# Kernel tuning notes

Measured on AMD Instinct MI355X. Metric: run time of the kernel, lower is better.

Reference implementation:

```python
import jax, jax.numpy as jnp
import numpy as np

N = 50000      # nodes
E = 800000     # edges (avg degree 16)
IN, HID, OUT = 256, 128, 64


def _glorot(key, shape):
    fan_in, fan_out = shape[0], shape[1]
    limit = np.sqrt(6.0 / (fan_in + fan_out))
    return jax.random.uniform(key, shape, jnp.float32, -limit, limit)


def setup_inputs() -> dict:
    key = jax.random.key(0)
    ks = jax.random.split(key, 8)
    x = jax.random.normal(ks[0], (N, IN), jnp.float32)
    edge_index = jax.random.randint(ks[1], (2, E), 0, N, dtype=jnp.int64)
    W1 = _glorot(ks[2], (IN, HID))
    b1 = jnp.zeros((HID,), jnp.float32)
    W2 = _glorot(ks[3], (HID, OUT))
    b2 = jnp.zeros((OUT,), jnp.float32)
    aw1 = _glorot(ks[4], (HID, 1))
    ab1 = jnp.zeros((1,), jnp.float32)
    aw2 = _glorot(ks[5], (OUT, 1))
    ab2 = jnp.zeros((1,), jnp.float32)
    return {"x": x, "edge_index": edge_index, "W1": W1, "b1": b1,
            "W2": W2, "b2": b2, "aw1": aw1, "ab1": ab1, "aw2": aw2, "ab2": ab2}


def gcn_conv(x, W, b, src, dst, n):
    # PyG GCNConv: add self-loops, symmetric degree normalization, then aggregate.
    h = x @ W                                   # [n, out]
    loops = jnp.arange(n, dtype=src.dtype)
    s = jnp.concatenate([src, loops])           # [E+n]
    d = jnp.concatenate([dst, loops])
    deg = jax.ops.segment_sum(jnp.ones(s.shape[0], h.dtype), d, num_segments=n)
    dinv = jnp.where(deg > 0, jax.lax.rsqrt(deg), 0.0)
    norm = dinv[s] * dinv[d]                    # [E+n]
    out = jax.ops.segment_sum(h[s] * norm[:, None], d, num_segments=n)
    return out + b


def reference(x, edge_index, W1, b1, W2, b2, aw1, ab1, aw2, ab2):
    # eval mode: dropout is identity
    src, dst = edge_index[0], edge_index[1]
    h = gcn_conv(x, W1, b1, src, dst, N)
    h = jax.nn.relu(h)
    h = h * jax.nn.sigmoid(h @ aw1 + ab1)       # sigmoid attention gate 1
    h = gcn_conv(h, W2, b2, src, dst, N)
    return h * jax.nn.sigmoid(h @ aw2 + ab2)    # sigmoid attention gate 2
```

## Files before the change

### kernel.cpp

```cpp
#include <hip/hip_runtime.h>
#include <math.h>

#define N_NODES 50000
#define N_EDGES 800000
#define D_IN    256
#define D_HID   128
#define D_OUT   64

#define NB 196
#define CH 2048
#define SLAB 4608

typedef unsigned int u32;
typedef unsigned short u16;
typedef __attribute__((ext_vector_type(8))) short bf16x8;
typedef __attribute__((ext_vector_type(4))) float f32x4;

__device__ __forceinline__ float bflo(u32 u) {
    union { u32 i; float f; } c; c.i = u << 16; return c.f;
}
__device__ __forceinline__ float bfhi(u32 u) {
    union { u32 i; float f; } c; c.i = u & 0xffff0000u; return c.f;
}
__device__ __forceinline__ u32 pack_bf2(float a, float b) {
    union { float f; u32 i; } ca, cb; ca.f = a; cb.f = b;
    u32 ra = (ca.i + 0x7fffu + ((ca.i >> 16) & 1u)) >> 16;
    u32 rb = (cb.i + 0x7fffu + ((cb.i >> 16) & 1u)) & 0xffff0000u;
    return ra | rb;
}

__device__ __forceinline__ int edge_at(const void* ei, int is64, int which, int i) {
    if (is64) return (int)((const long long*)ei)[(size_t)which * N_EDGES + i];
    return ((const int*)ei)[which * N_EDGES + i];
}

__device__ __forceinline__ int detect_is64(const void* ei, int t, int* s_is32) {
    if (t == 0) *s_is32 = 0;
    __syncthreads();
    if (t < 256) {
        int vv = ((const int*)ei)[2 * t + 1];
        if (vv != 0) atomicOr(s_is32, 1);
    }
    __syncthreads();
    return (*s_is32 == 0);
}


__global__ __launch_bounds__(256) void k_scatter1(const void* __restrict__ ei,
                                                  int* __restrict__ bcur,
                                                  u32* __restrict__ ebuf) {
    __shared__ int h[NB], gbase[NB], lc[NB];
    __shared__ int s_is32;
    int t = threadIdx.x;
    int is64 = detect_is64(ei, t, &s_is32);
    for (int i = t; i < NB; i += 256) { h[i] = 0; lc[i] = 0; }
    __syncthreads();
    int base = blockIdx.x * CH;

    u32 p[CH / 256];
    #pragma unroll
    for (int j = 0; j < CH / 256; ++j) {
        int i = base + j * 256 + t;
        if (i < N_EDGES) {
            int s = edge_at(ei, is64, 0, i);
            int d = edge_at(ei, is64, 1, i);
            p[j] = (u32)s | ((u32)d << 16);
            atomicAdd(&h[d >> 8], 1);
        }
    }
    __syncthreads();
    for (int i = t; i < NB; i += 256) if (h[i]) gbase[i] = atomicAdd(&bcur[i], h[i]);
    __syncthreads();
    #pragma unroll
    for (int j = 0; j < CH / 256; ++j) {
        int i = base + j * 256 + t;
        if (i < N_EDGES) {
            int b = (int)(p[j] >> 24);
            int lp = atomicAdd(&lc[b], 1);
            ebuf[gbase[b] + lp] = p[j];
        }
    }
}

__global__ __launch_bounds__(256) void k_scatter2(const u32* __restrict__ ebuf,
                                                  const int* __restrict__ bcur,
                                                  int* __restrict__ rowstart,
                                                  int* __restrict__ cnt,
                                                  float* __restrict__ dinv,
                                                  int* __restrict__ colidx) {
    __shared__ int h2[256], lofs[256], cur[256], sm[256];
    int b = blockIdx.x, t = threadIdx.x;
    int e0 = b * SLAB, ne = bcur[b] - e0;
    h2[t] = 0; cur[t] = 0;
    __syncthreads();
    for (int i = t; i < ne; i += 256) {
        u32 p = ebuf[e0 + i];
        atomicAdd(&h2[(p >> 16) & 255], 1);
    }
    __syncthreads();
    int v = h2[t]; sm[t] = v; __syncthreads();
    for (int off = 1; off < 256; off <<= 1) {
        int a = (t >= off) ? sm[t - off] : 0;
        __syncthreads();
        sm[t] += a;
        __syncthreads();
    }
    lofs[t] = sm[t] - v;
    __syncthreads();
    int node = (b << 8) + t;
    if (node < N_NODES) {
        rowstart[node] = e0 + lofs[t];
        cnt[node] = v;
        dinv[node] = rsqrtf(1.0f + (float)v);
    }
    for (int i = t; i < ne; i += 256) {
        u32 p = ebuf[e0 + i];
        int dl = (p >> 16) & 255;
        int lp = atomicAdd(&cur[dl], 1);
        colidx[e0 + lofs[dl] + lp] = (int)(p & 0xffffu);
    }
}

__global__ void k_wsplit(const float* __restrict__ W1, u16* __restrict__ t1h,
                         u16* __restrict__ t1l, const float* __restrict__ W2,
                         u16* __restrict__ t2h, u16* __restrict__ t2l,
                         int* __restrict__ bcur) {
    int i = blockIdx.x * 256 + threadIdx.x;
    if (i < NB) bcur[i] = i * SLAB;
    if (i < D_IN * D_HID) {
        int k = i / D_HID, c = i - k * D_HID;
        u32 bits = __float_as_uint(W1[i]);
        u32 hb = bits & 0xffff0000u;
        float lo = __uint_as_float(bits) - __uint_as_float(hb);
        t1h[(size_t)c * D_IN + k] = (u16)(hb >> 16);
        t1l[(size_t)c * D_IN + k] = (u16)(__float_as_uint(lo) >> 16);
    }
    int j = i - D_IN * D_HID;
    if (j >= 0 && j < D_HID * D_OUT) {
        int k = j / D_OUT, c = j - k * D_OUT;
        u32 bits = __float_as_uint(W2[j]);
        u32 hb = bits & 0xffff0000u;
        float lo = __uint_as_float(bits) - __uint_as_float(hb);
        t2h[(size_t)c * D_HID + k] = (u16)(hb >> 16);
        t2l[(size_t)c * D_HID + k] = (u16)(__float_as_uint(lo) >> 16);
    }
}

template <int K, int NF>
__global__ __launch_bounds__(256) void k_gemm_mfma(
    const float* __restrict__ A, const u16* __restrict__ tHi,
    const u16* __restrict__ tLo, const float* __restrict__ dinv,
    u32* __restrict__ Cp, int M) {
    constexpr int NT = NF / 16;
    constexpr int LDK = 40;
    __shared__ u16 aH[128][LDK], aL[128][LDK];
    __shared__ u16 wH[NF][LDK], wL[NF][LDK];

    const int t = threadIdx.x;
    const int lane = t & 63, wv = t >> 6;
    const int m0 = blockIdx.x * 128;
    const int lr = lane & 15, lk = (lane >> 4) * 8;

    f32x4 acc[2][NT] = {};

    const int arow = t >> 1;
    const int akq = (t & 1) * 16;
    const bool aok = (m0 + arow) < M;
    const float* asrc = A + (size_t)(m0 + arow) * K + akq;

    for (int ks = 0; ks < K; ks += 32) {
        {
            float f[16];
            #pragma unroll
            for (int j = 0; j < 16; ++j) f[j] = 0.0f;
            if (aok) {
                const float4* p = (const float4*)(asrc + ks);
                float4 v0 = p[0], v1 = p[1], v2 = p[2], v3 = p[3];
                f[0] = v0.x; f[1] = v0.y; f[2]  = v0.z; f[3]  = v0.w;
                f[4] = v1.x; f[5] = v1.y; f[6]  = v1.z; f[7]  = v1.w;
                f[8] = v2.x; f[9] = v2.y; f[10] = v2.z; f[11] = v2.w;
                f[12] = v3.x; f[13] = v3.y; f[14] = v3.z; f[15] = v3.w;
            }
            u32 hp[8], lp[8];
            #pragma unroll
            for (int q = 0; q < 8; ++q) {
                u32 b0 = __float_as_uint(f[2 * q]);
                u32 b1 = __float_as_uint(f[2 * q + 1]);
                u32 h0 = b0 & 0xffff0000u, h1 = b1 & 0xffff0000u;
                float l0 = f[2 * q] - __uint_as_float(h0);
                float l1 = f[2 * q + 1] - __uint_as_float(h1);
                hp[q] = (h0 >> 16) | h1;
                lp[q] = (__float_as_uint(l0) >> 16) | (__float_as_uint(l1) & 0xffff0000u);
            }
            *(uint4*)&aH[arow][akq + 0] = make_uint4(hp[0], hp[1], hp[2], hp[3]);
            *(uint4*)&aH[arow][akq + 8] = make_uint4(hp[4], hp[5], hp[6], hp[7]);
            *(uint4*)&aL[arow][akq + 0] = make_uint4(lp[0], lp[1], lp[2], lp[3]);
            *(uint4*)&aL[arow][akq + 8] = make_uint4(lp[4], lp[5], lp[6], lp[7]);
        }
        #pragma unroll
        for (int idx = t; idx < NF * 4; idx += 256) {
            int col = idx >> 2;
            int k8 = (idx & 3) * 8;
            *(uint4*)&wH[col][k8] = *(const uint4*)&tHi[(size_t)col * K + ks + k8];
            *(uint4*)&wL[col][k8] = *(const uint4*)&tLo[(size_t)col * K + ks + k8];
        }
        __syncthreads();

        bf16x8 afH[2], afL[2];
        #pragma unroll
        for (int mt = 0; mt < 2; ++mt) {
            int r = wv * 32 + mt * 16 + lr;
            afH[mt] = *(const bf16x8*)&aH[r][lk];
            afL[mt] = *(const bf16x8*)&aL[r][lk];
        }
        #pragma unroll
        for (int nt = 0; nt < NT; ++nt) {
            bf16x8 bh = *(const bf16x8*)&wH[nt * 16 + lr][lk];
            bf16x8 bl = *(const bf16x8*)&wL[nt * 16 + lr][lk];
            #pragma unroll
            for (int mt = 0; mt < 2; ++mt) {
                acc[mt][nt] = __builtin_amdgcn_mfma_f32_16x16x32_bf16(afH[mt], bh, acc[mt][nt], 0, 0, 0);
                acc[mt][nt] = __builtin_amdgcn_mfma_f32_16x16x32_bf16(afL[mt], bh, acc[mt][nt], 0, 0, 0);
                acc[mt][nt] = __builtin_amdgcn_mfma_f32_16x16x32_bf16(afH[mt], bl, acc[mt][nt], 0, 0, 0);
            }
        }
        __syncthreads();
    }

    #pragma unroll
    for (int mt = 0; mt < 2; ++mt) {
        #pragma unroll
        for (int r = 0; r < 4; ++r) {
            int row = m0 + wv * 32 + mt * 16 + (lane >> 4) * 4 + r;
            float dv = (row < M) ? dinv[row] : 0.0f;
            #pragma unroll
            for (int nt = 0; nt < NT; ++nt) {
                float v = acc[mt][nt][r] * dv;
                float vn = __shfl_xor(v, 1);
                if (!(lane & 1) && row < M) {
                    Cp[(size_t)row * (NF / 2) + nt * 8 + (lr >> 1)] = pack_bf2(v, vn);
                }
            }
        }
    }
}


__global__ __launch_bounds__(256) void k_agg1(
        const u32* __restrict__ hs, const int* __restrict__ rowstart,
        const int* __restrict__ cnt, const int* __restrict__ colidx,
        const float* __restrict__ dinv,
        const float* __restrict__ b, const float* __restrict__ aw,
        const float* __restrict__ ab, float* __restrict__ out) {
    int v = blockIdx.x * 4 + (threadIdx.x >> 6);
    int l = threadIdx.x & 63;
    if (v >= N_NODES) return;
    float dv = dinv[v];
    u32 su = hs[(size_t)v * 64 + l];
    float ax = bflo(su), ay = bfhi(su);
    int start = rowstart[v], len = cnt[v];
    const int* cx = colidx + start;
    int j = 0;
    for (; j + 8 <= len; j += 8) {
        int s0 = cx[j], s1 = cx[j + 1], s2 = cx[j + 2], s3 = cx[j + 3];
        int s4 = cx[j + 4], s5 = cx[j + 5], s6 = cx[j + 6], s7 = cx[j + 7];
        u32 u0 = hs[(size_t)s0 * 64 + l];
        u32 u1 = hs[(size_t)s1 * 64 + l];
        u32 u2 = hs[(size_t)s2 * 64 + l];
        u32 u3 = hs[(size_t)s3 * 64 + l];
        u32 u4 = hs[(size_t)s4 * 64 + l];
        u32 u5 = hs[(size_t)s5 * 64 + l];
        u32 u6 = hs[(size_t)s6 * 64 + l];
        u32 u7 = hs[(size_t)s7 * 64 + l];
        ax += bflo(u0) + bflo(u1) + bflo(u2) + bflo(u3)
            + bflo(u4) + bflo(u5) + bflo(u6) + bflo(u7);
        ay += bfhi(u0) + bfhi(u1) + bfhi(u2) + bfhi(u3)
            + bfhi(u4) + bfhi(u5) + bfhi(u6) + bfhi(u7);
    }
    for (; j + 4 <= len; j += 4) {
        int s0 = cx[j], s1 = cx[j + 1], s2 = cx[j + 2], s3 = cx[j + 3];
        u32 u0 = hs[(size_t)s0 * 64 + l];
        u32 u1 = hs[(size_t)s1 * 64 + l];
        u32 u2 = hs[(size_t)s2 * 64 + l];
        u32 u3 = hs[(size_t)s3 * 64 + l];
        ax += bflo(u0) + bflo(u1) + bflo(u2) + bflo(u3);
        ay += bfhi(u0) + bfhi(u1) + bfhi(u2) + bfhi(u3);
    }
    for (; j < len; ++j) {
        u32 u = hs[(size_t)cx[j] * 64 + l];
        ax += bflo(u); ay += bfhi(u);
    }
    float2 bp = ((const float2*)b)[l];
    ax = fmaxf(ax * dv + bp.x, 0.0f);
    ay = fmaxf(ay * dv + bp.y, 0.0f);
    float2 ap = ((const float2*)aw)[l];
    float p = ax * ap.x + ay * ap.y;
    for (int off = 32; off; off >>= 1) p += __shfl_xor(p, off);
    float g = 1.0f / (1.0f + expf(-(p + ab[0])));
    ((float2*)out)[(size_t)v * 64 + l] = make_float2(ax * g, ay * g);
}

__global__ __launch_bounds__(256) void k_agg2(
        const u32* __restrict__ hs, const int* __restrict__ rowstart,
        const int* __restrict__ cnt, const int* __restrict__ colidx,
        const float* __restrict__ dinv,
        const float* __restrict__ b, const float* __restrict__ aw,
        const float* __restrict__ ab, float* __restrict__ out) {
    int v = blockIdx.x * 4 + (threadIdx.x >> 6);
    int l = threadIdx.x & 63;
    if (v >= N_NODES) return;
    int c = l & 31, half = l >> 5;
    float dv = dinv[v];
    float ax = 0.0f, ay = 0.0f;
    if (half == 0) {
        u32 su = hs[(size_t)v * 32 + c];
        ax = bflo(su); ay = bfhi(su);
    }
    int start = rowstart[v], len = cnt[v];
    const int* cx = colidx + start;
    int j = half;
    for (; j + 6 < len; j += 8) {
        int s0 = cx[j], s1 = cx[j + 2], s2 = cx[j + 4], s3 = cx[j + 6];
        u32 u0 = hs[(size_t)s0 * 32 + c];
        u32 u1 = hs[(size_t)s1 * 32 + c];
        u32 u2 = hs[(size_t)s2 * 32 + c];
        u32 u3 = hs[(size_t)s3 * 32 + c];
        ax += bflo(u0) + bflo(u1) + bflo(u2) + bflo(u3);
        ay += bfhi(u0) + bfhi(u1) + bfhi(u2) + bfhi(u3);
    }
    for (; j + 2 < len; j += 4) {
        int s0 = cx[j], s1 = cx[j + 2];
        u32 u0 = hs[(size_t)s0 * 32 + c];
        u32 u1 = hs[(size_t)s1 * 32 + c];
        ax += bflo(u0) + bflo(u1);
        ay += bfhi(u0) + bfhi(u1);
    }
    if (j < len) {
        u32 u = hs[(size_t)cx[j] * 32 + c];
        ax += bflo(u); ay += bfhi(u);
    }
    ax += __shfl_xor(ax, 32);
    ay += __shfl_xor(ay, 32);
    float2 bp = ((const float2*)b)[c];
    ax = ax * dv + bp.x;
    ay = ay * dv + bp.y;
    float2 ap = ((const float2*)aw)[c];
    float p = ax * ap.x + ay * ap.y;
    for (int off = 16; off; off >>= 1) p += __shfl_xor(p, off);
    float g = 1.0f / (1.0f + expf(-(p + ab[0])));
    if (half == 0) ((float2*)out)[(size_t)v * 32 + c] = make_float2(ax * g, ay * g);
}


static inline size_t align_up(size_t x, size_t a) { return (x + a - 1) & ~(a - 1); }

extern "C" void kernel_launch(void* const* d_in, const int* in_sizes, int n_in,
                              void* d_out, int out_size, void* d_ws, size_t ws_size,
                              hipStream_t stream) {
    const float* x   = (const float*)d_in[0];
    const void*  ei  = d_in[1];
    const float* W1  = (const float*)d_in[2];
    const float* b1  = (const float*)d_in[3];
    const float* W2  = (const float*)d_in[4];
    const float* b2  = (const float*)d_in[5];
    const float* aw1 = (const float*)d_in[6];
    const float* ab1 = (const float*)d_in[7];
    const float* aw2 = (const float*)d_in[8];
    const float* ab2 = (const float*)d_in[9];
    float* out = (float*)d_out;

    char* w = (char*)d_ws;
    size_t off = 0;
    int*   bcur     = (int*)(w + off); off = align_up(off + NB * 4, 256);
    int*   cnt      = (int*)(w + off); off = align_up(off + N_NODES * 4, 256);
    int*   rowstart = (int*)(w + off); off = align_up(off + N_NODES * 4, 256);
    float* dinv     = (float*)(w + off); off = align_up(off + N_NODES * 4, 256);
    u32*   ebuf     = (u32*)(w + off); off = align_up(off + (size_t)NB * SLAB * 4, 256);
    int*   colidx   = (int*)(w + off); off = align_up(off + (size_t)NB * SLAB * 4, 256);
    u32*   h1s      = (u32*)(w + off); off = align_up(off + (size_t)N_NODES * 64 * 4, 256);
    float* h1g      = (float*)(w + off); off = align_up(off + (size_t)N_NODES * D_HID * 4, 256);
    u32*   h2s      = (u32*)(w + off); off = align_up(off + (size_t)N_NODES * 32 * 4, 256);
    u16*   wt1h     = (u16*)(w + off); off = align_up(off + (size_t)D_IN * D_HID * 2, 256);
    u16*   wt1l     = (u16*)(w + off); off = align_up(off + (size_t)D_IN * D_HID * 2, 256);
    u16*   wt2h     = (u16*)(w + off); off = align_up(off + (size_t)D_HID * D_OUT * 2, 256);
    u16*   wt2l     = (u16*)(w + off); off = align_up(off + (size_t)D_HID * D_OUT * 2, 256);
    (void)ws_size; (void)out_size; (void)n_in; (void)in_sizes;

    k_wsplit<<<(D_IN * D_HID + D_HID * D_OUT + 255) / 256, 256, 0, stream>>>(
        W1, wt1h, wt1l, W2, wt2h, wt2l, bcur);

    k_scatter1<<<(N_EDGES + CH - 1) / CH, 256, 0, stream>>>(ei, bcur, ebuf);
    k_scatter2<<<NB, 256, 0, stream>>>(ebuf, bcur, rowstart, cnt, dinv, colidx);

    k_gemm_mfma<D_IN, D_HID><<<(N_NODES + 127) / 128, 256, 0, stream>>>(
        x, wt1h, wt1l, dinv, h1s, N_NODES);
    k_agg1<<<(N_NODES + 3) / 4, 256, 0, stream>>>(
        h1s, rowstart, cnt, colidx, dinv, b1, aw1, ab1, h1g);

    k_gemm_mfma<D_HID, D_OUT><<<(N_NODES + 127) / 128, 256, 0, stream>>>(
        h1g, wt2h, wt2l, dinv, h2s, N_NODES);
    k_agg2<<<(N_NODES + 3) / 4, 256, 0, stream>>>(
        h2s, rowstart, cnt, colidx, dinv, b2, aw2, ab2, out);
}
```

Measured before the change: 225.8 us.

## Fuse second-layer GEMM into first aggregation kernel via shared-memory W2

The first aggregation kernel now also applies the second layer's linear transform. Each block loads a transposed fp32 W2 into shared memory, and each wave multiplies its gated 128-wide hidden row by W2 on CUDA cores, then scales by dinv. The result is written directly as packed bf16 h2s. This drops the fp32 h1g round trip (50000x128 floats) and the separate MFMA GEMM launch. In exchange, each block adds 32KB of shared-memory W2 staging, a 128-long scalar dot product per output lane, and block size 512, which may lower occupancy for the latency-bound gather. Removing the bounds check assumes N is divisible by 8.

```diff
diff --git a/kernel.cpp b/kernel.cpp
--- a/kernel.cpp
+++ b/kernel.cpp
@@ -123,8 +123,7 @@
 
 __global__ void k_wsplit(const float* __restrict__ W1, u16* __restrict__ t1h,
                          u16* __restrict__ t1l, const float* __restrict__ W2,
-                         u16* __restrict__ t2h, u16* __restrict__ t2l,
-                         int* __restrict__ bcur) {
+                         float* __restrict__ w2tg, int* __restrict__ bcur) {
     int i = blockIdx.x * 256 + threadIdx.x;
     if (i < NB) bcur[i] = i * SLAB;
     if (i < D_IN * D_HID) {
@@ -137,12 +136,8 @@
     }
     int j = i - D_IN * D_HID;
     if (j >= 0 && j < D_HID * D_OUT) {
-        int k = j / D_OUT, c = j - k * D_OUT;
-        u32 bits = __float_as_uint(W2[j]);
-        u32 hb = bits & 0xffff0000u;
-        float lo = __uint_as_float(bits) - __uint_as_float(hb);
-        t2h[(size_t)c * D_HID + k] = (u16)(hb >> 16);
-        t2l[(size_t)c * D_HID + k] = (u16)(__float_as_uint(lo) >> 16);
+        int k = j / D_OUT, f = j - k * D_OUT;
+        w2tg[f * D_HID + k] = W2[j];
     }
 }
 
@@ -245,16 +240,24 @@
     }
 }
 
-
-__global__ __launch_bounds__(256) void k_agg1(
+__global__ __launch_bounds__(512) void k_agg1g(
         const u32* __restrict__ hs, const int* __restrict__ rowstart,
         const int* __restrict__ cnt, const int* __restrict__ colidx,
         const float* __restrict__ dinv,
         const float* __restrict__ b, const float* __restrict__ aw,
-        const float* __restrict__ ab, float* __restrict__ out) {
-    int v = blockIdx.x * 4 + (threadIdx.x >> 6);
-    int l = threadIdx.x & 63;
-    if (v >= N_NODES) return;
+        const float* __restrict__ ab, const float* __restrict__ w2tg,
+        u32* __restrict__ h2s) {
+    __shared__ float w2t[64 * 130];
+    __shared__ float hbuf[8][128];
+    int t = threadIdx.x;
+    for (int i = t; i < 64 * 128; i += 512) {
+        int f = i >> 7, k = i & 127;
+        w2t[f * 130 + k] = w2tg[i];
+    }
+    __syncthreads();
+
+    int wv = t >> 6, l = t & 63;
+    int v = blockIdx.x * 8 + wv;
     float dv = dinv[v];
     u32 su = hs[(size_t)v * 64 + l];
     float ax = bflo(su), ay = bfhi(su);
@@ -297,7 +300,23 @@
     float p = ax * ap.x + ay * ap.y;
     for (int off = 32; off; off >>= 1) p += __shfl_xor(p, off);
     float g = 1.0f / (1.0f + expf(-(p + ab[0])));
-    ((float2*)out)[(size_t)v * 64 + l] = make_float2(ax * g, ay * g);
+
+    *(float2*)&hbuf[wv][2 * l] = make_float2(ax * g, ay * g);
+
+    float o0 = 0.0f, o1 = 0.0f;
+    const float* wrow = &w2t[l * 130];
+    #pragma unroll 8
+    for (int k2 = 0; k2 < 64; k2 += 2) {
+        float2 h0 = *(const float2*)&hbuf[wv][2 * k2];
+        float2 h1 = *(const float2*)&hbuf[wv][2 * k2 + 2];
+        float2 w0 = *(const float2*)&wrow[2 * k2];
+        float2 w1 = *(const float2*)&wrow[2 * k2 + 2];
+        o0 += h0.x * w0.x + h0.y * w0.y;
+        o1 += h1.x * w1.x + h1.y * w1.y;
+    }
+    float o = (o0 + o1) * dv;
+    float on = __shfl_xor(o, 1);
+    if (!(l & 1)) h2s[(size_t)v * 32 + (l >> 1)] = pack_bf2(o, on);
 }
 
 __global__ __launch_bounds__(256) void k_agg2(
@@ -378,27 +397,24 @@
     u32*   ebuf     = (u32*)(w + off); off = align_up(off + (size_t)NB * SLAB * 4, 256);
     int*   colidx   = (int*)(w + off); off = align_up(off + (size_t)NB * SLAB * 4, 256);
     u32*   h1s      = (u32*)(w + off); off = align_up(off + (size_t)N_NODES * 64 * 4, 256);
-    float* h1g      = (float*)(w + off); off = align_up(off + (size_t)N_NODES * D_HID * 4, 256);
     u32*   h2s      = (u32*)(w + off); off = align_up(off + (size_t)N_NODES * 32 * 4, 256);
     u16*   wt1h     = (u16*)(w + off); off = align_up(off + (size_t)D_IN * D_HID * 2, 256);
     u16*   wt1l     = (u16*)(w + off); off = align_up(off + (size_t)D_IN * D_HID * 2, 256);
-    u16*   wt2h     = (u16*)(w + off); off = align_up(off + (size_t)D_HID * D_OUT * 2, 256);
-    u16*   wt2l     = (u16*)(w + off); off = align_up(off + (size_t)D_HID * D_OUT * 2, 256);
+    float* w2tg     = (float*)(w + off); off = align_up(off + (size_t)D_OUT * D_HID * 4, 256);
     (void)ws_size; (void)out_size; (void)n_in; (void)in_sizes;
 
     k_wsplit<<<(D_IN * D_HID + D_HID * D_OUT + 255) / 256, 256, 0, stream>>>(
-        W1, wt1h, wt1l, W2, wt2h, wt2l, bcur);
+        W1, wt1h, wt1l, W2, w2tg, bcur);
 
     k_scatter1<<<(N_EDGES + CH - 1) / CH, 256, 0, stream>>>(ei, bcur, ebuf);
     k_scatter2<<<NB, 256, 0, stream>>>(ebuf, bcur, rowstart, cnt, dinv, colidx);
 
     k_gemm_mfma<D_IN, D_HID><<<(N_NODES + 127) / 128, 256, 0, stream>>>(
         x, wt1h, wt1l, dinv, h1s, N_NODES);
-    k_agg1<<<(N_NODES + 3) / 4, 256, 0, stream>>>(
-        h1s, rowstart, cnt, colidx, dinv, b1, aw1, ab1, h1g);
-
-    k_gemm_mfma<D_HID, D_OUT><<<(N_NODES + 127) / 128, 256, 0, stream>>>(
-        h1g, wt2h, wt2l, dinv, h2s, N_NODES);
+
+    k_agg1g<<<N_NODES / 8, 512, 0, stream>>>(
+        h1s, rowstart, cnt, colidx, dinv, b1, aw1, ab1, w2tg, h2s);
+
     k_agg2<<<(N_NODES + 3) / 4, 256, 0, stream>>>(
         h2s, rowstart, cnt, colidx, dinv, b2, aw2, ab2, out);
 }
```

Measured after the change: 248.0 us. 1.1x slower.
